# Performance work log

Measured on AMD Instinct MI355X. Metric: run time of the kernel, lower is better.

## Reference

```python
import jax, jax.numpy as jnp
import numpy as np

LN_EPS = 1e-5


def setup_inputs() -> dict:
    key = jax.random.key(0)
    ks = jax.random.split(key, 4)
    B, N, C, K = 512, 100, 256, 3
    query = jax.random.normal(ks[0], (B, N, C), dtype=jnp.float32)
    value = jax.random.normal(ks[1], (B, N, C), dtype=jnp.float32)
    # nn.Linear(C, N+K): weight stored as [out,in] in torch; here use [in,out]
    W_wl = jax.random.normal(ks[2], (C, N + K), dtype=jnp.float32) / np.sqrt(C)
    b_wl = jax.random.normal(ks[3], (N + K,), dtype=jnp.float32) * 0.01
    ln_gamma = jnp.ones((C,), dtype=jnp.float32)
    ln_beta = jnp.zeros((C,), dtype=jnp.float32)
    return {"query": query, "value": value, "W_wl": W_wl, "b_wl": b_wl,
            "ln_gamma": ln_gamma, "ln_beta": ln_beta}


def reference(query, value, W_wl, b_wl, ln_gamma, ln_beta):
    B, N, C = query.shape
    K = W_wl.shape[1] - N
    # dynamic conv weights from query: [B, N, K] depthwise + [B, N, N] pointwise
    dy = jnp.einsum('bnc,ck->bnk', query, W_wl) + b_wl
    dw = dy[:, :, :K]          # depthwise kernels, one per (b, proposal)
    pw = dy[:, :, K:]          # pointwise mixing matrix [B, N, N]
    # depthwise conv1d along C with 'same' padding (cross-correlation like torch)
    pad_l = (K - 1) // 2
    pad_r = K - 1 - pad_l
    vp = jnp.pad(value, ((0, 0), (0, 0), (pad_l, pad_r)))
    depth = jnp.zeros_like(value)
    for k in range(K):  # K is tiny (3): static unrolled loop
        depth = depth + dw[:, :, k:k + 1] * vp[:, :, k:k + C]
    depth = jax.nn.relu(depth)
    # pointwise conv (kernel size 1) == per-sample NxN mix over proposals
    out = jnp.einsum('bnm,bmc->bnc', pw, depth)
    # LayerNorm over C
    mu = jnp.mean(out, axis=-1, keepdims=True)
    var = jnp.var(out, axis=-1, keepdims=True)
    out = (out - mu) * jax.lax.rsqrt(var + LN_EPS) * ln_gamma + ln_beta
    return out
```

## Files before the change

### kernel.cpp

```cpp
#include <hip/hip_runtime.h>

#define NN 100
#define CC 256
#define NKK 103
#define LSA 72
#define LDPW 136
#define OTS 260

typedef __bf16 bf16;
typedef __bf16 bf16x4 __attribute__((ext_vector_type(4)));
typedef __bf16 bf16x8 __attribute__((ext_vector_type(8)));
typedef float f32x4 __attribute__((ext_vector_type(4)));

__global__ void wl_transpose(const float* __restrict__ W, bf16* __restrict__ Wt)
{
    int idx = blockIdx.x * 256 + threadIdx.x;
    if (idx < NKK * CC) {
        int ka = idx >> 8;
        int k  = idx & 255;
        Wt[ka * CC + k] = (bf16)W[k * NKK + ka];
    }
}

__global__ __launch_bounds__(512, 4)
void dysepconv_fused(const float* __restrict__ query,
                     const float* __restrict__ value,
                     const bf16*  __restrict__ Wt,
                     const float* __restrict__ bwl,
                     const float* __restrict__ gamma,
                     const float* __restrict__ beta,
                     float* __restrict__ out)
{
    __shared__ __align__(16) char SMEM[50000];
    bf16*  PW   = (bf16*)SMEM;
    bf16*  Abuf = (bf16*)(SMEM + 27200);
    float (*DW)[3]      = (float(*)[3])(SMEM + 41600);
    float (*RP)[NN][2]  = (float(*)[NN][2])(SMEM + 42800);
    float (*RS)[2]      = (float(*)[2])(SMEM + 49200);
    float* OT = (float*)SMEM;

    const int t    = threadIdx.x;
    const int w    = t >> 6;
    const int lane = t & 63;
    const int ln16 = lane & 15;
    const int g    = lane >> 4;
    const int hi8  = g * 8;
    const int b    = blockIdx.x;
    const int cb   = w * 16 + ln16;

    const float* qb = query + (size_t)b * NN * CC;
    const float* vb = value + (size_t)b * NN * CC;

    f32x4 acc1[7];
    #pragma unroll
    for (int I = 0; I < 7; ++I) acc1[I] = (f32x4){0.f, 0.f, 0.f, 0.f};

    const int rB = (w * 16 + ln16 < NKK) ? (w * 16 + ln16) : (NKK - 1);

    f32x4 qv[4];
    #pragma unroll
    for (int p = 0; p < 4; ++p) {
        int idx = p * 512 + t;
        if (idx < 1600) {
            int r = idx >> 4, j = (idx & 15) << 2;
            qv[p] = *(const f32x4*)(qb + r * CC + j);
        }
    }

    #pragma unroll
    for (int kc = 0; kc < 4; ++kc) {
        if (kc) __syncthreads();
        #pragma unroll
        for (int p = 0; p < 4; ++p) {
            int idx = p * 512 + t;
            if (idx < 1600) {
                int r = idx >> 4, j = (idx & 15) << 2;
                bf16x4 s;
                #pragma unroll
                for (int i = 0; i < 4; ++i) s[i] = (bf16)qv[p][i];
                *(bf16x4*)&Abuf[r * LSA + j] = s;
            }
        }
        bf16x8 wf0 = *(const bf16x8*)(Wt + rB * CC + kc * 64 + hi8);
        bf16x8 wf1 = *(const bf16x8*)(Wt + rB * CC + kc * 64 + 32 + hi8);
        f32x4 qn[4];
        if (kc < 3) {
            #pragma unroll
            for (int p = 0; p < 4; ++p) {
                int idx = p * 512 + t;
                if (idx < 1600) {
                    int r = idx >> 4, j = (idx & 15) << 2;
                    qn[p] = *(const f32x4*)(qb + r * CC + (kc + 1) * 64 + j);
                }
            }
        }
        __syncthreads();

        if (w < 7) {
            #pragma unroll
            for (int I = 0; I < 7; ++I) {
                int row = I * 16 + ln16;
                row = (row < NN) ? row : (NN - 1);
                bf16x8 av = *(const bf16x8*)&Abuf[row * LSA + hi8];
                acc1[I] = __builtin_amdgcn_mfma_f32_16x16x32_bf16(av, wf0, acc1[I], 0, 0, 0);
            }
            #pragma unroll
            for (int I = 0; I < 7; ++I) {
                int row = I * 16 + ln16;
                row = (row < NN) ? row : (NN - 1);
                bf16x8 av = *(const bf16x8*)&Abuf[row * LSA + 32 + hi8];
                acc1[I] = __builtin_amdgcn_mfma_f32_16x16x32_bf16(av, wf1, acc1[I], 0, 0, 0);
            }
        }
        if (kc < 3) {
            #pragma unroll
            for (int p = 0; p < 4; ++p) qv[p] = qn[p];
        }
    }

    for (int i = t; i < NN * 28; i += 512) {
        int r = i / 28, m = 100 + (i - (i / 28) * 28);
        PW[r * LDPW + m] = (bf16)0.f;
    }
    float xv[8], yv[8];
    #pragma unroll
    for (int j = 0; j < 8; ++j) {
        int m = hi8 + j;
        const float* vr = vb + m * CC;
        xv[j] = vr[cb];
        yv[j] = vr[cb + 128];
    }
    if (w < 7) {
        const int kap = w * 16 + ln16;
        const float bw = (kap < NKK) ? bwl[kap] : 0.f;
        #pragma unroll
        for (int I = 0; I < 7; ++I) {
            #pragma unroll
            for (int r = 0; r < 4; ++r) {
                int n = I * 16 + g * 4 + r;
                if (n < NN && kap < NKK) {
                    float v = acc1[I][r] + bw;
                    if (kap < 3) DW[n][kap] = v;
                    else         PW[n * LDPW + (kap - 3)] = (bf16)v;
                }
            }
        }
    }
    __syncthreads();

    f32x4 acc2[2][7];
    #pragma unroll
    for (int st = 0; st < 2; ++st)
        #pragma unroll
        for (int I = 0; I < 7; ++I) acc2[st][I] = (f32x4){0.f, 0.f, 0.f, 0.f};

    #pragma unroll
    for (int ks = 0; ks < 4; ++ks) {
        if (ks) {
            #pragma unroll
            for (int j = 0; j < 8; ++j) {
                int m = ks * 32 + hi8 + j;
                bool mv = (m < NN);
                const float* vr = vb + m * CC;
                xv[j] = mv ? vr[cb]       : 0.f;
                yv[j] = mv ? vr[cb + 128] : 0.f;
            }
        }
        bf16x8 dv0, dv1;
        #pragma unroll
        for (int j = 0; j < 8; ++j) {
            int  m  = ks * 32 + hi8 + j;
            bool mv = (m < NN);
            int  mc = mv ? m : (NN - 1);
            float w0 = DW[mc][0], w1 = DW[mc][1], w2 = DW[mc][2];
            float x0 = xv[j], y0 = yv[j];
            float xm = __shfl(x0, (lane - 1) & 63), xp = __shfl(x0, (lane + 1) & 63);
            float ym = __shfl(y0, (lane - 1) & 63), yp = __shfl(y0, (lane + 1) & 63);
            if (ln16 == 0) {
                xm = (mv && cb > 0) ? vb[m * CC + cb - 1] : 0.f;
                ym = mv ? vb[m * CC + cb + 127] : 0.f;
            }
            if (ln16 == 15) {
                xp = mv ? vb[m * CC + cb + 1] : 0.f;
                yp = (mv && cb + 129 < CC) ? vb[m * CC + cb + 129] : 0.f;
            }
            float d0 = w0 * xm + w1 * x0 + w2 * xp;
            float d1 = w0 * ym + w1 * y0 + w2 * yp;
            dv0[j] = (bf16)(mv ? fmaxf(d0, 0.f) : 0.f);
            dv1[j] = (bf16)(mv ? fmaxf(d1, 0.f) : 0.f);
        }
        #pragma unroll
        for (int I = 0; I < 7; ++I) {
            int row = I * 16 + ln16;
            row = (row < NN) ? row : (NN - 1);
            bf16x8 af = *(const bf16x8*)&PW[row * LDPW + ks * 32 + hi8];
            acc2[0][I] = __builtin_amdgcn_mfma_f32_16x16x32_bf16(af, dv0, acc2[0][I], 0, 0, 0);
            acc2[1][I] = __builtin_amdgcn_mfma_f32_16x16x32_bf16(af, dv1, acc2[1][I], 0, 0, 0);
        }
    }

    const float gm0 = gamma[cb], gm1 = gamma[cb + 128];
    const float bt0 = beta[cb],  bt1 = beta[cb + 128];

    #pragma unroll
    for (int I = 0; I < 7; ++I) {
        #pragma unroll
        for (int r = 0; r < 4; ++r) {
            float a = acc2[0][I][r], e = acc2[1][I][r];
            float s1 = a + e, s2 = a * a + e * e;
            #pragma unroll
            for (int mk = 1; mk < 16; mk <<= 1) {
                s1 += __shfl_xor(s1, mk);
                s2 += __shfl_xor(s2, mk);
            }
            int n = I * 16 + g * 4 + r;
            if (ln16 == 0 && n < NN) {
                RP[w][n][0] = s1;
                RP[w][n][1] = s2;
            }
        }
    }
    __syncthreads();
    if (t < NN) {
        float S1 = 0.f, S2 = 0.f;
        #pragma unroll
        for (int wi = 0; wi < 8; ++wi) { S1 += RP[wi][t][0]; S2 += RP[wi][t][1]; }
        float mu  = S1 * (1.f / 256.f);
        float var = S2 * (1.f / 256.f) - mu * mu;
        RS[t][0] = mu;
        RS[t][1] = rsqrtf(fmaxf(var, 0.f) + 1e-5f);
    }
    __syncthreads();

    float* ob = out + (size_t)b * NN * CC;
    #pragma unroll
    for (int h = 0; h < 3; ++h) {
        const int n0   = h * 40;
        const int rows = (h == 2) ? 20 : 40;
        #pragma unroll
        for (int I = 0; I < 7; ++I) {
            #pragma unroll
            for (int r = 0; r < 4; ++r) {
                int n = I * 16 + g * 4 + r;
                if (n >= n0 && n < n0 + rows) {
                    float mu = RS[n][0], rs = RS[n][1];
                    int rt = n - n0;
                    OT[rt * OTS + cb]       = (acc2[0][I][r] - mu) * rs * gm0 + bt0;
                    OT[rt * OTS + cb + 128] = (acc2[1][I][r] - mu) * rs * gm1 + bt1;
                }
            }
        }
        __syncthreads();
        #pragma unroll
        for (int p = 0; p < 5; ++p) {
            int idx = p * 512 + t;
            if (idx < rows * 64) {
                int row = idx >> 6, c4 = (idx & 63) << 2;
                *(f32x4*)(ob + (size_t)(n0 + row) * CC + c4) = *(const f32x4*)&OT[row * OTS + c4];
            }
        }
        if (h < 2) __syncthreads();
    }
}

extern "C" void kernel_launch(void* const* d_in, const int* in_sizes, int n_in,
                              void* d_out, int out_size, void* d_ws, size_t ws_size,
                              hipStream_t stream) {
    const float* query = (const float*)d_in[0];
    const float* value = (const float*)d_in[1];
    const float* W     = (const float*)d_in[2];
    const float* bwl   = (const float*)d_in[3];
    const float* gamma = (const float*)d_in[4];
    const float* beta  = (const float*)d_in[5];
    bf16* Wt = (bf16*)d_ws;

    wl_transpose<<<dim3((NKK * CC + 255) / 256), dim3(256), 0, stream>>>(W, Wt);
    dysepconv_fused<<<dim3(512), dim3(512), 0, stream>>>(query, value, Wt, bwl, gamma, beta, (float*)d_out);
}
```

Measured before the change: 189.6 us.

## Load query A-fragments directly from global, swap GEMM1 tiling, add sched barriers

The first GEMM no longer stages bf16 query tiles in shared memory with block-wide syncs. Each wave now loads its own 16 query rows straight from global into A fragments and loops over all 7 output-column tiles, reading W fragments from global/L2. This drops the LDS staging buffer and four barriers but rereads the weights per wave. The epilogue writes output in two 50-row halves instead of three chunks, and sched_barrier hints are added to split the MFMA and conv instruction streams.

```diff
diff --git a/kernel.cpp b/kernel.cpp
--- a/kernel.cpp
+++ b/kernel.cpp
@@ -3,7 +3,6 @@
 #define NN 100
 #define CC 256
 #define NKK 103
-#define LSA 72
 #define LDPW 136
 #define OTS 260
 
@@ -31,12 +30,11 @@
                      const float* __restrict__ beta,
                      float* __restrict__ out)
 {
-    __shared__ __align__(16) char SMEM[50000];
-    bf16*  PW   = (bf16*)SMEM;
-    bf16*  Abuf = (bf16*)(SMEM + 27200);
-    float (*DW)[3]      = (float(*)[3])(SMEM + 41600);
-    float (*RP)[NN][2]  = (float(*)[NN][2])(SMEM + 42800);
-    float (*RS)[2]      = (float(*)[2])(SMEM + 49200);
+    __shared__ __align__(16) char SMEM[52800];
+    bf16*  PW = (bf16*)SMEM;
+    float (*DW)[3]     = (float(*)[3])(SMEM + 27200);
+    float (*RP)[NN][2] = (float(*)[NN][2])(SMEM + 28400);
+    float (*RS)[2]     = (float(*)[2])(SMEM + 52000);
     float* OT = (float*)SMEM;
 
     const int t    = threadIdx.x;
@@ -53,68 +51,30 @@
 
     f32x4 acc1[7];
     #pragma unroll
-    for (int I = 0; I < 7; ++I) acc1[I] = (f32x4){0.f, 0.f, 0.f, 0.f};
-
-    const int rB = (w * 16 + ln16 < NKK) ? (w * 16 + ln16) : (NKK - 1);
-
-    f32x4 qv[4];
-    #pragma unroll
-    for (int p = 0; p < 4; ++p) {
-        int idx = p * 512 + t;
-        if (idx < 1600) {
-            int r = idx >> 4, j = (idx & 15) << 2;
-            qv[p] = *(const f32x4*)(qb + r * CC + j);
-        }
-    }
-
-    #pragma unroll
-    for (int kc = 0; kc < 4; ++kc) {
-        if (kc) __syncthreads();
-        #pragma unroll
-        for (int p = 0; p < 4; ++p) {
-            int idx = p * 512 + t;
-            if (idx < 1600) {
-                int r = idx >> 4, j = (idx & 15) << 2;
-                bf16x4 s;
+    for (int J = 0; J < 7; ++J) acc1[J] = (f32x4){0.f, 0.f, 0.f, 0.f};
+
+    if (w < 7) {
+        const int qrow = (w * 16 + ln16 < NN) ? (w * 16 + ln16) : (NN - 1);
+        const float* qr = qb + qrow * CC;
+        #pragma unroll
+        for (int kc = 0; kc < 4; ++kc) {
+            bf16x8 qf[2];
+            #pragma unroll
+            for (int s = 0; s < 2; ++s) {
+                f32x4 a0 = *(const f32x4*)(qr + kc * 64 + s * 32 + hi8);
+                f32x4 a1 = *(const f32x4*)(qr + kc * 64 + s * 32 + hi8 + 4);
                 #pragma unroll
-                for (int i = 0; i < 4; ++i) s[i] = (bf16)qv[p][i];
-                *(bf16x4*)&Abuf[r * LSA + j] = s;
-            }
-        }
-        bf16x8 wf0 = *(const bf16x8*)(Wt + rB * CC + kc * 64 + hi8);
-        bf16x8 wf1 = *(const bf16x8*)(Wt + rB * CC + kc * 64 + 32 + hi8);
-        f32x4 qn[4];
-        if (kc < 3) {
-            #pragma unroll
-            for (int p = 0; p < 4; ++p) {
-                int idx = p * 512 + t;
-                if (idx < 1600) {
-                    int r = idx >> 4, j = (idx & 15) << 2;
-                    qn[p] = *(const f32x4*)(qb + r * CC + (kc + 1) * 64 + j);
-                }
-            }
-        }
-        __syncthreads();
-
-        if (w < 7) {
-            #pragma unroll
-            for (int I = 0; I < 7; ++I) {
-                int row = I * 16 + ln16;
-                row = (row < NN) ? row : (NN - 1);
-                bf16x8 av = *(const bf16x8*)&Abuf[row * LSA + hi8];
-                acc1[I] = __builtin_amdgcn_mfma_f32_16x16x32_bf16(av, wf0, acc1[I], 0, 0, 0);
-            }
-            #pragma unroll
-            for (int I = 0; I < 7; ++I) {
-                int row = I * 16 + ln16;
-                row = (row < NN) ? row : (NN - 1);
-                bf16x8 av = *(const bf16x8*)&Abuf[row * LSA + 32 + hi8];
-                acc1[I] = __builtin_amdgcn_mfma_f32_16x16x32_bf16(av, wf1, acc1[I], 0, 0, 0);
-            }
-        }
-        if (kc < 3) {
-            #pragma unroll
-            for (int p = 0; p < 4; ++p) qv[p] = qn[p];
+                for (int i = 0; i < 4; ++i) { qf[s][i] = (bf16)a0[i]; qf[s][i + 4] = (bf16)a1[i]; }
+            }
+            #pragma unroll
+            for (int J = 0; J < 7; ++J) {
+                const int rB = (J * 16 + ln16 < NKK) ? (J * 16 + ln16) : (NKK - 1);
+                bf16x8 bv0 = *(const bf16x8*)(Wt + rB * CC + kc * 64 + hi8);
+                bf16x8 bv1 = *(const bf16x8*)(Wt + rB * CC + kc * 64 + 32 + hi8);
+                acc1[J] = __builtin_amdgcn_mfma_f32_16x16x32_bf16(qf[0], bv0, acc1[J], 0, 0, 0);
+                acc1[J] = __builtin_amdgcn_mfma_f32_16x16x32_bf16(qf[1], bv1, acc1[J], 0, 0, 0);
+                if (J == 3) __builtin_amdgcn_sched_barrier(0);
+            }
         }
     }
 
@@ -131,15 +91,15 @@
         yv[j] = vr[cb + 128];
     }
     if (w < 7) {
-        const int kap = w * 16 + ln16;
-        const float bw = (kap < NKK) ? bwl[kap] : 0.f;
-        #pragma unroll
-        for (int I = 0; I < 7; ++I) {
+        #pragma unroll
+        for (int J = 0; J < 7; ++J) {
+            int kap = J * 16 + ln16;
+            float bw = (kap < NKK) ? bwl[kap] : 0.f;
             #pragma unroll
             for (int r = 0; r < 4; ++r) {
-                int n = I * 16 + g * 4 + r;
+                int n = w * 16 + g * 4 + r;
                 if (n < NN && kap < NKK) {
-                    float v = acc1[I][r] + bw;
+                    float v = acc1[J][r] + bw;
                     if (kap < 3) DW[n][kap] = v;
                     else         PW[n * LDPW + (kap - 3)] = (bf16)v;
                 }
@@ -188,6 +148,7 @@
             float d1 = w0 * ym + w1 * y0 + w2 * yp;
             dv0[j] = (bf16)(mv ? fmaxf(d0, 0.f) : 0.f);
             dv1[j] = (bf16)(mv ? fmaxf(d1, 0.f) : 0.f);
+            if (j == 3) __builtin_amdgcn_sched_barrier(0);
         }
         #pragma unroll
         for (int I = 0; I < 7; ++I) {
@@ -196,6 +157,7 @@
             bf16x8 af = *(const bf16x8*)&PW[row * LDPW + ks * 32 + hi8];
             acc2[0][I] = __builtin_amdgcn_mfma_f32_16x16x32_bf16(af, dv0, acc2[0][I], 0, 0, 0);
             acc2[1][I] = __builtin_amdgcn_mfma_f32_16x16x32_bf16(af, dv1, acc2[1][I], 0, 0, 0);
+            if (I == 3) __builtin_amdgcn_sched_barrier(0);
         }
     }
 
@@ -234,15 +196,14 @@
 
     float* ob = out + (size_t)b * NN * CC;
     #pragma unroll
-    for (int h = 0; h < 3; ++h) {
-        const int n0   = h * 40;
-        const int rows = (h == 2) ? 20 : 40;
+    for (int h = 0; h < 2; ++h) {
+        const int n0 = h * 50;
         #pragma unroll
         for (int I = 0; I < 7; ++I) {
             #pragma unroll
             for (int r = 0; r < 4; ++r) {
                 int n = I * 16 + g * 4 + r;
-                if (n >= n0 && n < n0 + rows) {
+                if (n >= n0 && n < n0 + 50 && n < NN) {
                     float mu = RS[n][0], rs = RS[n][1];
                     int rt = n - n0;
                     OT[rt * OTS + cb]       = (acc2[0][I][r] - mu) * rs * gm0 + bt0;
@@ -252,14 +213,14 @@
         }
         __syncthreads();
         #pragma unroll
-        for (int p = 0; p < 5; ++p) {
+        for (int p = 0; p < 7; ++p) {
             int idx = p * 512 + t;
-            if (idx < rows * 64) {
+            if (idx < 50 * 64) {
                 int row = idx >> 6, c4 = (idx & 63) << 2;
                 *(f32x4*)(ob + (size_t)(n0 + row) * CC + c4) = *(const f32x4*)&OT[row * OTS + c4];
             }
         }
-        if (h < 2) __syncthreads();
+        if (h == 0) __syncthreads();
     }
 }
 
```

New measurement: 195.6 us. 3.2% more time.
